# Kernel optimization log

Measured on AMD Instinct MI355X. Metric: run time of the kernel, lower is better.

## Reference

```python
import jax, jax.numpy as jnp
import numpy as np

B = 256        # number of graphs
NPG = 256      # nodes per graph
N = B * NPG    # total nodes
F = 128        # node feature dim
DEG = 16       # avg degree
E = N * DEG    # total edges
LAT = [32, 32, 32, 1]
D = sum(LAT)   # total_latent_dim = 97
K = 30         # sortpool k
C1, C2, KW2 = 16, 32, 5
DENSE = ((K - 2) // 2 + 1 - KW2 + 1) * C2  # 352
OUT = 2


def setup_inputs() -> dict:
    key = jax.random.key(0)
    ks = jax.random.split(key, 16)
    node_feat = jax.random.normal(ks[0], (N, F), jnp.float32)
    # edges constrained within each graph (block-diagonal adjacency)
    base = ((jnp.arange(E, dtype=jnp.int32) // (E // B)) * NPG).astype(jnp.int32)
    src = jax.random.randint(ks[1], (E,), 0, NPG, dtype=jnp.int32) + base
    dst = jax.random.randint(ks[2], (E,), 0, NPG, dtype=jnp.int32) + base
    degs = jnp.zeros((N,), jnp.int32).at[dst].add(1)  # in-degree per node
    s = 0.1
    dims = [F] + LAT
    inp = {"node_feat": node_feat, "src": src, "dst": dst, "degs": degs}
    for i in range(4):
        inp[f"W{i}"] = jax.random.normal(ks[3 + i], (dims[i], dims[i + 1]), jnp.float32) * s
        inp[f"b{i}"] = jnp.zeros((dims[i + 1],), jnp.float32)
    inp["conv1_w"] = jax.random.normal(ks[8], (C1, 1, D), jnp.float32) * s
    inp["conv1_b"] = jnp.zeros((C1,), jnp.float32)
    inp["conv2_w"] = jax.random.normal(ks[9], (C2, C1, KW2), jnp.float32) * s
    inp["conv2_b"] = jnp.zeros((C2,), jnp.float32)
    inp["out_w"] = jax.random.normal(ks[10], (DENSE, OUT), jnp.float32) * s
    inp["out_b"] = jnp.zeros((OUT,), jnp.float32)
    return inp


def reference(node_feat, W0, b0, W1, b1, W2, b2, W3, b3,
              conv1_w, conv1_b, conv2_w, conv2_b, out_w, out_b,
              src, dst, degs):
    n = node_feat.shape[0]
    deg1 = (degs.astype(node_feat.dtype) + 1.0)[:, None]  # node_degs = deg + 1
    h = node_feat
    feats = []
    for W, b in ((W0, b0), (W1, b1), (W2, b2), (W3, b3)):
        # gnn_spmm(n2n, h) + h : sparse adjacency matmul via segment add
        pooled = jnp.zeros((n, h.shape[1]), h.dtype).at[dst].add(h[src]) + h
        h = jnp.tanh((pooled @ W + b) / deg1)
        feats.append(h)
    Z = jnp.concatenate(feats, axis=1)          # [N, D]
    Zb = Z.reshape(B, NPG, D)                   # equal-sized graphs
    # sortpooling: top-k on last latent channel per graph, gather rows
    _, idx = jax.lax.top_k(Zb[:, :, -1], K)     # [B, K]
    sp = jnp.take_along_axis(Zb, idx[:, :, None], axis=1)  # [B, K, D]
    x = sp.reshape(B, 1, K * D)
    dn = ('NCH', 'OIH', 'NCH')
    x = jax.lax.conv_general_dilated(x, conv1_w, (D,), 'VALID', dimension_numbers=dn)
    x = jax.nn.relu(x + conv1_b[None, :, None])          # [B, C1, K]
    x = x.reshape(B, C1, K // 2, 2).max(axis=-1)         # maxpool1d(2,2) -> [B, C1, 15]
    x = jax.lax.conv_general_dilated(x, conv2_w, (1,), 'VALID', dimension_numbers=dn)
    x = jax.nn.relu(x + conv2_b[None, :, None])          # [B, C2, 11]
    to_dense = x.reshape(B, -1)                          # [B, 352]
    out = jax.nn.relu(to_dense @ out_w + out_b)
    return jax.nn.relu(out)  # original applies conv1d_activation twice at the end
```

## Files before the change

### kernel.cpp

```cpp
#include <hip/hip_runtime.h>

#define NPG  256
#define EPG  4096
#define FDIM 128
#define KTOP 30

__global__ __launch_bounds__(512)
__attribute__((amdgpu_waves_per_eu(2, 2)))
void dgcnn_fused(const float* __restrict__ node_feat,
                 const int* __restrict__ srcv, const int* __restrict__ dstv,
                 const int* __restrict__ degs,
                 const float* __restrict__ W0, const float* __restrict__ b0,
                 const float* __restrict__ W1, const float* __restrict__ b1,
                 const float* __restrict__ W2, const float* __restrict__ b2,
                 const float* __restrict__ W3, const float* __restrict__ b3,
                 const float* __restrict__ cw1, const float* __restrict__ cb1,
                 const float* __restrict__ cw2, const float* __restrict__ cb2,
                 const float* __restrict__ ow,  const float* __restrict__ ob,
                 float* __restrict__ outp)
{
    __shared__ float Ybuf[NPG * 33];
    __shared__ int   srclist[EPG];
    __shared__ int   offs[NPG];
    __shared__ int   cnt [NPG];
    __shared__ int   degl[NPG];
    __shared__ float invd[NPG];
    __shared__ float keys[NPG];
    __shared__ int   wsum[4];

    const int g    = blockIdx.x;
    const int t    = threadIdx.x;
    const int n    = t & (NPG - 1);
    const int half = t >> 8;
    const int co   = half * 16;

    const int dn = degs[g * NPG + n];
    if (half == 0) {
        degl[n] = dn;
        cnt[n]  = 0;
        invd[n] = 1.0f / (float)(dn + 1);
    }
    {
        int v = (half == 0) ? dn : 0;
        const int lane = t & 63;
        #pragma unroll
        for (int off = 1; off < 64; off <<= 1) {
            int u = __shfl_up(v, off);
            if (lane >= off) v += u;
        }
        if (half == 0 && lane == 63) wsum[t >> 6] = v;
        __syncthreads();
        if (half == 0) {
            const int w = t >> 6;
            int base = 0;
            #pragma unroll
            for (int i = 0; i < 4; i++) base += (i < w) ? wsum[i] : 0;
            offs[n] = base + v - dn;
        }
        __syncthreads();
    }

    {
        const int* sg = srcv + g * EPG;
        const int* dg = dstv + g * EPG;
        #pragma unroll
        for (int i = 0; i < EPG / 512; i++) {
            int e  = t + i * 512;
            int ss = sg[e] & (NPG - 1);
            int dd = dg[e] & (NPG - 1);
            int p  = atomicAdd(&cnt[dd], 1);
            srclist[offs[dd] + p] = ss;
        }
    }

    {
        const float* nf  = node_feat + ((size_t)g * NPG + n) * FDIM + half * 64;
        const float4* nf4 = (const float4*)nf;
        const int kb = half * 64;

        float acc[32];
        #pragma unroll
        for (int c = 0; c < 32; c++) acc[c] = 0.f;

        auto fma4 = [&](float4 r, int kbase) {
            const float* w0 = W0 + (kbase + 0) * 32;
            const float* w1 = W0 + (kbase + 1) * 32;
            const float* w2 = W0 + (kbase + 2) * 32;
            const float* w3 = W0 + (kbase + 3) * 32;
            #pragma unroll
            for (int c = 0; c < 32; c++) {
                float a = acc[c];
                a = fmaf(r.x, w0[c], a);
                a = fmaf(r.y, w1[c], a);
                a = fmaf(r.z, w2[c], a);
                a = fmaf(r.w, w3[c], a);
                acc[c] = a;
            }
        };

        float4 a0 = nf4[0],  a1 = nf4[1],  a2 = nf4[2],  a3 = nf4[3];
        float4 b0 = nf4[4],  b1 = nf4[5],  b2 = nf4[6],  b3 = nf4[7];
        fma4(a0, kb + 0);  fma4(a1, kb + 4);  fma4(a2, kb + 8);  fma4(a3, kb + 12);
        a0 = nf4[8];  a1 = nf4[9];  a2 = nf4[10]; a3 = nf4[11];
        fma4(b0, kb + 16); fma4(b1, kb + 20); fma4(b2, kb + 24); fma4(b3, kb + 28);
        b0 = nf4[12]; b1 = nf4[13]; b2 = nf4[14]; b3 = nf4[15];
        fma4(a0, kb + 32); fma4(a1, kb + 36); fma4(a2, kb + 40); fma4(a3, kb + 44);
        fma4(b0, kb + 48); fma4(b1, kb + 52); fma4(b2, kb + 56); fma4(b3, kb + 60);

        __syncthreads();
        if (half == 0) {
            #pragma unroll
            for (int c = 0; c < 32; c++) Ybuf[n * 33 + c] = acc[c];
        }
        __syncthreads();
        if (half == 1) {
            #pragma unroll
            for (int c = 0; c < 32; c++) Ybuf[n * 33 + c] += acc[c];
        }
        __syncthreads();
    }

    const float iv = invd[n];
    const int   o  = offs[n];
    const int   d  = degl[n];

    auto agg16 = [&](float (&h)[16]) {
        const float* self = &Ybuf[n * 33 + co];
        #pragma unroll
        for (int c = 0; c < 16; c++) h[c] = self[c];
        for (int j = 0; j < d; j++) {
            const float* yr = &Ybuf[srclist[o + j] * 33 + co];
            #pragma unroll
            for (int c = 0; c < 16; c++) h[c] += yr[c];
        }
    };
    auto act16 = [&](float (&h)[16], const float* bb) {
        #pragma unroll
        for (int c = 0; c < 16; c++) h[c] = tanhf((h[c] + bb[co + c]) * iv);
    };
    auto matml16 = [&](const float (&h)[16], const float* Wn) {
        float a[32];
        #pragma unroll
        for (int c = 0; c < 32; c++) a[c] = 0.f;
        #pragma unroll
        for (int kk = 0; kk < 16; kk++) {
            const float* wr = Wn + (co + kk) * 32;
            const float  hk = h[kk];
            #pragma unroll
            for (int c = 0; c < 32; c++) a[c] = fmaf(hk, wr[c], a[c]);
        }
        __syncthreads();
        if (half == 0) {
            #pragma unroll
            for (int c = 0; c < 32; c++) Ybuf[n * 33 + c] = a[c];
        }
        __syncthreads();
        if (half == 1) {
            #pragma unroll
            for (int c = 0; c < 32; c++) Ybuf[n * 33 + c] += a[c];
        }
        __syncthreads();
    };

    float h1[16], h2[16], h3[16];
    agg16(h1); act16(h1, b0); matml16(h1, W1);
    agg16(h2); act16(h2, b1); matml16(h2, W2);
    agg16(h3); act16(h3, b2);
    {
        float a3 = 0.f;
        #pragma unroll
        for (int kk = 0; kk < 16; kk++) a3 = fmaf(h3[kk], W3[co + kk], a3);
        __syncthreads();
        if (half == 0) Ybuf[n * 33] = a3;
        __syncthreads();
        if (half == 1) Ybuf[n * 33] += a3;
        __syncthreads();
    }
    float kv;
    {
        float s = Ybuf[n * 33];
        for (int j = 0; j < d; j++) s += Ybuf[srclist[o + j] * 33];
        kv = tanhf((s + b3[0]) * iv);
        if (half == 0) keys[n] = kv;
    }
    __syncthreads();

    int rank = 0;
    #pragma unroll 4
    for (int j = 0; j < NPG; j++) {
        float vj = keys[j];
        rank += ((vj > kv) || ((vj == kv) && (j < n))) ? 1 : 0;
    }

    float* sp    = (float*)srclist;
    float* x1    = sp + 30 * 97;
    float* xp    = x1 + 480;
    float* dense = xp + 240;

    if (rank < KTOP) {
        float* dp = sp + rank * 97 + co;
        #pragma unroll
        for (int c = 0; c < 16; c++) dp[c]      = h1[c];
        #pragma unroll
        for (int c = 0; c < 16; c++) dp[32 + c] = h2[c];
        #pragma unroll
        for (int c = 0; c < 16; c++) dp[64 + c] = h3[c];
        if (half == 0) sp[rank * 97 + 96] = kv;
    }
    __syncthreads();

    for (int idx = t; idx < 480; idx += 512) {
        int k = idx >> 4, c = idx & 15;
        float s = cb1[c];
        for (int dd = 0; dd < 97; dd++) s = fmaf(sp[k * 97 + dd], cw1[c * 97 + dd], s);
        x1[c * 30 + k] = fmaxf(s, 0.f);
    }
    __syncthreads();
    for (int idx = t; idx < 240; idx += 512) {
        int c = idx / 15, k = idx - c * 15;
        xp[idx] = fmaxf(x1[c * 30 + 2 * k], x1[c * 30 + 2 * k + 1]);
    }
    __syncthreads();
    for (int idx = t; idx < 352; idx += 512) {
        int c = idx / 11, j = idx - c * 11;
        float s = cb2[c];
        for (int i2 = 0; i2 < 16; i2++) {
            #pragma unroll
            for (int tt = 0; tt < 5; tt++)
                s = fmaf(xp[i2 * 15 + j + tt], cw2[(c * 16 + i2) * 5 + tt], s);
        }
        dense[idx] = fmaxf(s, 0.f);
    }
    __syncthreads();
    if (t < 64) {
        float a0 = 0.f, a1 = 0.f;
        for (int dd = t; dd < 352; dd += 64) {
            float v = dense[dd];
            a0 = fmaf(v, ow[dd * 2],     a0);
            a1 = fmaf(v, ow[dd * 2 + 1], a1);
        }
        #pragma unroll
        for (int off2 = 32; off2 > 0; off2 >>= 1) {
            a0 += __shfl_down(a0, off2);
            a1 += __shfl_down(a1, off2);
        }
        if (t == 0) {
            outp[g * 2 + 0] = fmaxf(a0 + ob[0], 0.f);
            outp[g * 2 + 1] = fmaxf(a1 + ob[1], 0.f);
        }
    }
}

extern "C" void kernel_launch(void* const* d_in, const int* in_sizes, int n_in,
                              void* d_out, int out_size, void* d_ws, size_t ws_size,
                              hipStream_t stream) {
    const float* node_feat = (const float*)d_in[0];
    const int*   src       = (const int*)  d_in[1];
    const int*   dst       = (const int*)  d_in[2];
    const int*   degsp     = (const int*)  d_in[3];
    const float* W0 = (const float*)d_in[4];
    const float* b0 = (const float*)d_in[5];
    const float* W1 = (const float*)d_in[6];
    const float* b1 = (const float*)d_in[7];
    const float* W2 = (const float*)d_in[8];
    const float* b2 = (const float*)d_in[9];
    const float* W3 = (const float*)d_in[10];
    const float* b3 = (const float*)d_in[11];
    const float* cw1 = (const float*)d_in[12];
    const float* cb1 = (const float*)d_in[13];
    const float* cw2 = (const float*)d_in[14];
    const float* cb2 = (const float*)d_in[15];
    const float* ow  = (const float*)d_in[16];
    const float* ob  = (const float*)d_in[17];

    dgcnn_fused<<<dim3(256), dim3(512), 0, stream>>>(
        node_feat, src, dst, degsp,
        W0, b0, W1, b1, W2, b2, W3, b3,
        cw1, cb1, cw2, cb2, ow, ob, (float*)d_out);
}
```

Measured before the change: 205.5 us.

## Split matmuls by output columns across halves instead of K-split reductions

The work split between the two thread halves changes from a K-split with a two-phase shared-memory reduction to an output-column split. Each half now computes 16 of the 32 output columns over the full input, so the first-layer matmul reads all 128 features per thread. Later layers exchange activations through shared memory and use a spare column for the last layer. This removes the serialized store-then-add phases, but adds shared-memory reads of the partner half's activations and doubles the node-feature global loads per node.

```diff
diff --git a/kernel.cpp b/kernel.cpp
--- a/kernel.cpp
+++ b/kernel.cpp
@@ -33,6 +33,7 @@
     const int n    = t & (NPG - 1);
     const int half = t >> 8;
     const int co   = half * 16;
+    const int oco  = co ^ 16;
 
     const int dn = degs[g * NPG + n];
     if (half == 0) {
@@ -74,21 +75,19 @@
     }
 
     {
-        const float* nf  = node_feat + ((size_t)g * NPG + n) * FDIM + half * 64;
-        const float4* nf4 = (const float4*)nf;
-        const int kb = half * 64;
-
-        float acc[32];
-        #pragma unroll
-        for (int c = 0; c < 32; c++) acc[c] = 0.f;
-
-        auto fma4 = [&](float4 r, int kbase) {
-            const float* w0 = W0 + (kbase + 0) * 32;
-            const float* w1 = W0 + (kbase + 1) * 32;
-            const float* w2 = W0 + (kbase + 2) * 32;
-            const float* w3 = W0 + (kbase + 3) * 32;
-            #pragma unroll
-            for (int c = 0; c < 32; c++) {
+        const float4* nf4 = (const float4*)(node_feat + ((size_t)g * NPG + n) * FDIM);
+        float acc[16];
+        #pragma unroll
+        for (int c = 0; c < 16; c++) acc[c] = 0.f;
+        #pragma unroll 4
+        for (int q = 0; q < 32; q++) {
+            const float4 r = nf4[q];
+            const float* w0 = W0 + (q * 4 + 0) * 32 + co;
+            const float* w1 = W0 + (q * 4 + 1) * 32 + co;
+            const float* w2 = W0 + (q * 4 + 2) * 32 + co;
+            const float* w3 = W0 + (q * 4 + 3) * 32 + co;
+            #pragma unroll
+            for (int c = 0; c < 16; c++) {
                 float a = acc[c];
                 a = fmaf(r.x, w0[c], a);
                 a = fmaf(r.y, w1[c], a);
@@ -96,27 +95,9 @@
                 a = fmaf(r.w, w3[c], a);
                 acc[c] = a;
             }
-        };
-
-        float4 a0 = nf4[0],  a1 = nf4[1],  a2 = nf4[2],  a3 = nf4[3];
-        float4 b0 = nf4[4],  b1 = nf4[5],  b2 = nf4[6],  b3 = nf4[7];
-        fma4(a0, kb + 0);  fma4(a1, kb + 4);  fma4(a2, kb + 8);  fma4(a3, kb + 12);
-        a0 = nf4[8];  a1 = nf4[9];  a2 = nf4[10]; a3 = nf4[11];
-        fma4(b0, kb + 16); fma4(b1, kb + 20); fma4(b2, kb + 24); fma4(b3, kb + 28);
-        b0 = nf4[12]; b1 = nf4[13]; b2 = nf4[14]; b3 = nf4[15];
-        fma4(a0, kb + 32); fma4(a1, kb + 36); fma4(a2, kb + 40); fma4(a3, kb + 44);
-        fma4(b0, kb + 48); fma4(b1, kb + 52); fma4(b2, kb + 56); fma4(b3, kb + 60);
-
-        __syncthreads();
-        if (half == 0) {
-            #pragma unroll
-            for (int c = 0; c < 32; c++) Ybuf[n * 33 + c] = acc[c];
-        }
-        __syncthreads();
-        if (half == 1) {
-            #pragma unroll
-            for (int c = 0; c < 32; c++) Ybuf[n * 33 + c] += acc[c];
-        }
+        }
+        #pragma unroll
+        for (int c = 0; c < 16; c++) Ybuf[n * 33 + co + c] = acc[c];
         __syncthreads();
     }
 
@@ -138,48 +119,62 @@
         #pragma unroll
         for (int c = 0; c < 16; c++) h[c] = tanhf((h[c] + bb[co + c]) * iv);
     };
+    auto store_h = [&](const float (&h)[16]) {
+        #pragma unroll
+        for (int c = 0; c < 16; c++) Ybuf[n * 33 + co + c] = h[c];
+    };
     auto matml16 = [&](const float (&h)[16], const float* Wn) {
-        float a[32];
-        #pragma unroll
-        for (int c = 0; c < 32; c++) a[c] = 0.f;
+        float a[16];
+        #pragma unroll
+        for (int c = 0; c < 16; c++) a[c] = 0.f;
         #pragma unroll
         for (int kk = 0; kk < 16; kk++) {
-            const float* wr = Wn + (co + kk) * 32;
+            const float* wr = Wn + (co + kk) * 32 + co;
             const float  hk = h[kk];
             #pragma unroll
-            for (int c = 0; c < 32; c++) a[c] = fmaf(hk, wr[c], a[c]);
-        }
-        __syncthreads();
-        if (half == 0) {
-            #pragma unroll
-            for (int c = 0; c < 32; c++) Ybuf[n * 33 + c] = a[c];
-        }
-        __syncthreads();
-        if (half == 1) {
-            #pragma unroll
-            for (int c = 0; c < 32; c++) Ybuf[n * 33 + c] += a[c];
-        }
+            for (int c = 0; c < 16; c++) a[c] = fmaf(hk, wr[c], a[c]);
+        }
+        #pragma unroll
+        for (int kk = 0; kk < 16; kk++) {
+            const float* wr = Wn + (oco + kk) * 32 + co;
+            const float  hk = Ybuf[n * 33 + oco + kk];
+            #pragma unroll
+            for (int c = 0; c < 16; c++) a[c] = fmaf(hk, wr[c], a[c]);
+        }
+        __syncthreads();
+        #pragma unroll
+        for (int c = 0; c < 16; c++) Ybuf[n * 33 + co + c] = a[c];
         __syncthreads();
     };
 
     float h1[16], h2[16], h3[16];
-    agg16(h1); act16(h1, b0); matml16(h1, W1);
-    agg16(h2); act16(h2, b1); matml16(h2, W2);
+    agg16(h1); act16(h1, b0);
+    __syncthreads();
+    store_h(h1);
+    __syncthreads();
+    matml16(h1, W1);
+
+    agg16(h2); act16(h2, b1);
+    __syncthreads();
+    store_h(h2);
+    __syncthreads();
+    matml16(h2, W2);
+
     agg16(h3); act16(h3, b2);
+    __syncthreads();
+    store_h(h3);
+    __syncthreads();
+    float kv;
     {
         float a3 = 0.f;
         #pragma unroll
         for (int kk = 0; kk < 16; kk++) a3 = fmaf(h3[kk], W3[co + kk], a3);
-        __syncthreads();
-        if (half == 0) Ybuf[n * 33] = a3;
-        __syncthreads();
-        if (half == 1) Ybuf[n * 33] += a3;
-        __syncthreads();
-    }
-    float kv;
-    {
-        float s = Ybuf[n * 33];
-        for (int j = 0; j < d; j++) s += Ybuf[srclist[o + j] * 33];
+        #pragma unroll
+        for (int kk = 0; kk < 16; kk++) a3 = fmaf(Ybuf[n * 33 + oco + kk], W3[oco + kk], a3);
+        if (half == 0) Ybuf[n * 33 + 32] = a3;
+        __syncthreads();
+        float s = Ybuf[n * 33 + 32];
+        for (int j = 0; j < d; j++) s += Ybuf[srclist[o + j] * 33 + 32];
         kv = tanhf((s + b3[0]) * iv);
         if (half == 0) keys[n] = kv;
     }
```

Result: slower. 210.6 us (+2.5%).
